# Kernel optimization log

Measured on AMD Instinct MI355X. Metric: run time of the kernel, lower is better.

The kernel has to match this reference:

```python
import jax, jax.numpy as jnp
import numpy as np

NUM_HEADS = 8


def _conv1(x, w, b):
    # 1x1x1 Conv3d == per-voxel channel linear map. x: [B,C,D,H,W], w: [O,C], b: [O]
    return jnp.einsum('bcdhw,oc->bodhw', x, w) + b[None, :, None, None, None]


def setup_inputs() -> dict:
    key = jax.random.key(0)
    ks = jax.random.split(key, 7)
    B, C, D, H, W = 1, 64, 16, 16, 16
    s = 0.02
    return {
        'decoder_features': jax.random.normal(ks[0], (B, C, D, H, W), jnp.float32),
        'mae_features': jax.random.normal(ks[1], (B, C, D, H, W), jnp.float32),
        'q_w': jax.random.normal(ks[2], (C, C), jnp.float32) * s,
        'q_b': jnp.zeros((C,), jnp.float32),
        'k_w': jax.random.normal(ks[3], (C, C), jnp.float32) * s,
        'k_b': jnp.zeros((C,), jnp.float32),
        'v_w': jax.random.normal(ks[4], (C, C), jnp.float32) * s,
        'v_b': jnp.zeros((C,), jnp.float32),
        'o_w': jax.random.normal(ks[5], (C, C), jnp.float32) * s,
        'o_b': jnp.zeros((C,), jnp.float32),
    }


def reference(decoder_features, mae_features, q_w, q_b, k_w, k_b, v_w, v_b, o_w, o_b):
    B, C, D, H, W = decoder_features.shape
    nh = NUM_HEADS
    hd = C // nh
    N = D * H * W
    scale = hd ** -0.5

    def split_heads(x):
        # [B,C,D,H,W] -> [B, nh, N, hd]
        return x.reshape(B, nh, hd, N).transpose(0, 1, 3, 2)

    Q = split_heads(_conv1(decoder_features, q_w, q_b))
    K = split_heads(_conv1(mae_features, k_w, k_b))
    V = split_heads(_conv1(mae_features, v_w, v_b))

    attn = jax.nn.softmax(jnp.einsum('bhnc,bhmc->bhnm', Q, K) * scale, axis=-1)
    out = jnp.einsum('bhnm,bhmc->bhnc', attn, V)  # [B, nh, N, hd]
    out = out.transpose(0, 1, 3, 2).reshape(B, C, D, H, W)
    return _conv1(out, o_w, o_b)
```

## Files before the change

kernel.cpp:

```cpp
#include <hip/hip_runtime.h>
#include <hip/hip_bf16.h>
#include <math.h>


#define N_VOX 4096
#define NH 8
#define QSCALE 0.51010813f

typedef unsigned short ushort_t;
typedef __attribute__((ext_vector_type(8))) short bf16x8;
typedef __attribute__((ext_vector_type(16))) float f32x16;

__device__ __forceinline__ unsigned short f2bf(float f) {
  union { float f; unsigned u; } v; v.f = f;
  unsigned r = v.u + 0x7FFFu + ((v.u >> 16) & 1u);
  return (unsigned short)(r >> 16);
}
__device__ __forceinline__ unsigned pk2bf(float a, float b) {
  __hip_bfloat162 h = __float22bfloat162_rn(float2{a, b});
  union { __hip_bfloat162 h; unsigned u; } c; c.h = h;
  return c.u;
}
__device__ __forceinline__ float ex2(float x) { return __builtin_amdgcn_exp2f(x); }

__global__ __launch_bounds__(256) void qkv_pack(
    const float* __restrict__ dec, const float* __restrict__ mae,
    const float* __restrict__ qw, const float* __restrict__ qb_,
    const float* __restrict__ kw, const float* __restrict__ kb,
    const float* __restrict__ vw, const float* __restrict__ vb,
    ushort_t* __restrict__ Qp, ushort_t* __restrict__ Kp,
    ushort_t* __restrict__ Vt, ushort_t* __restrict__ zeroblk) {
  const int bx = blockIdx.x;
  const int n = blockIdx.y * 256 + threadIdx.x;

  if (bx < 8) {
    const int h = bx;
    float x[64];
#pragma unroll
    for (int c = 0; c < 64; ++c) x[c] = dec[c * N_VOX + n];
    float qv[8];
#pragma unroll
    for (int j = 0; j < 8; ++j) {
      const int o = h * 8 + j;
      float a = qb_[o];
#pragma unroll
      for (int c = 0; c < 64; ++c) a = fmaf(x[c], qw[o * 64 + c], a);
      qv[j] = a * QSCALE;
    }
    uint4 pk;
    pk.x = pk2bf(qv[0], qv[1]); pk.y = pk2bf(qv[2], qv[3]);
    pk.z = pk2bf(qv[4], qv[5]); pk.w = pk2bf(qv[6], qv[7]);
    *(uint4*)(Qp + ((size_t)h * N_VOX + n) * 8) = pk;
  } else {
    const int h = bx - 8;
    float x[64];
#pragma unroll
    for (int c = 0; c < 64; ++c) x[c] = mae[c * N_VOX + n];
    float kv[8], vv[8];
#pragma unroll
    for (int j = 0; j < 8; ++j) {
      const int o = h * 8 + j;
      float a = kb[o], b = vb[o];
#pragma unroll
      for (int c = 0; c < 64; ++c) {
        a = fmaf(x[c], kw[o * 64 + c], a);
        b = fmaf(x[c], vw[o * 64 + c], b);
      }
      kv[j] = a; vv[j] = b;
    }
    uint4 pk;
    pk.x = pk2bf(kv[0], kv[1]); pk.y = pk2bf(kv[2], kv[3]);
    pk.z = pk2bf(kv[4], kv[5]); pk.w = pk2bf(kv[6], kv[7]);
    *(uint4*)(Kp + ((size_t)h * N_VOX + n) * 8) = pk;
#pragma unroll
    for (int d = 0; d < 8; ++d)
      Vt[((size_t)(h * 32 + d)) * N_VOX + n] = f2bf(vv[d]);
    Vt[((size_t)(h * 32 + 8)) * N_VOX + n] = 0x3F80;
    if (h == 0 && n < 8) zeroblk[n] = 0;
  }
}

__global__ __launch_bounds__(256, 3) void attn_mfma(
    const ushort_t* __restrict__ Qp, const ushort_t* __restrict__ Kp,
    const ushort_t* __restrict__ Vt, const ushort_t* __restrict__ zeroblk,
    float* __restrict__ o_part, int kps) {
  const int tid = threadIdx.x;
  const int lane = tid & 63;
  const int wave = tid >> 6;
  const int l31 = lane & 31;
  const int lhalf = lane >> 5;
  const int h = blockIdx.y;
  const int ks = blockIdx.z;
  const int qb = blockIdx.x * 256 + wave * 64;

  __shared__ ushort_t P_lds[8][32 * 36];

  bf16x8 qfrag0 = *(const bf16x8*)(Qp + ((size_t)h * N_VOX + qb + l31) * 8);
  bf16x8 qfrag1 = *(const bf16x8*)(Qp + ((size_t)h * N_VOX + qb + 32 + l31) * 8);

  f32x16 zf, acc0, acc1;
#pragma unroll
  for (int i = 0; i < 16; ++i) { zf[i] = 0.f; acc0[i] = 0.f; acc1[i] = 0.f; }

  const ushort_t* KpH = Kp + (size_t)h * N_VOX * 8;
  const ushort_t* VtH = Vt + ((size_t)h * 32 + l31) * N_VOX;
  ushort_t* pb0 = &P_lds[wave * 2 + 0][l31 * 36];
  ushort_t* pb1 = &P_lds[wave * 2 + 1][l31 * 36];

  const int kbeg = ks * kps;
  for (int kk = 0; kk < kps; kk += 32) {
    const int kcur = kbeg + kk;
    const ushort_t* kp = lhalf ? zeroblk : (KpH + (size_t)(kcur + l31) * 8);
    bf16x8 kf = *(const bf16x8*)kp;

    f32x16 s0 = __builtin_amdgcn_mfma_f32_32x32x16_bf16(kf, qfrag0, zf, 0, 0, 0);
    f32x16 s1 = __builtin_amdgcn_mfma_f32_32x32x16_bf16(kf, qfrag1, zf, 0, 0, 0);

    bf16x8 vf0 = *(const bf16x8*)(VtH + kcur + lhalf * 8);
    bf16x8 vf1 = *(const bf16x8*)(VtH + kcur + 16 + lhalf * 8);

#pragma unroll
    for (int G = 0; G < 4; ++G) {
      uint2 w;
      w.x = pk2bf(ex2(s0[G * 4 + 0]), ex2(s0[G * 4 + 1]));
      w.y = pk2bf(ex2(s0[G * 4 + 2]), ex2(s0[G * 4 + 3]));
      *(uint2*)(pb0 + G * 8 + lhalf * 4) = w;
    }
#pragma unroll
    for (int G = 0; G < 4; ++G) {
      uint2 w;
      w.x = pk2bf(ex2(s1[G * 4 + 0]), ex2(s1[G * 4 + 1]));
      w.y = pk2bf(ex2(s1[G * 4 + 2]), ex2(s1[G * 4 + 3]));
      *(uint2*)(pb1 + G * 8 + lhalf * 4) = w;
    }

#pragma unroll
    for (int grp = 0; grp < 2; ++grp) {
      union { bf16x8 v; uint2 u[2]; } p0, p1;
      p0.u[0] = *(const uint2*)(pb0 + grp * 16 + lhalf * 8);
      p0.u[1] = *(const uint2*)(pb0 + grp * 16 + lhalf * 8 + 4);
      p1.u[0] = *(const uint2*)(pb1 + grp * 16 + lhalf * 8);
      p1.u[1] = *(const uint2*)(pb1 + grp * 16 + lhalf * 8 + 4);
      const bf16x8 vf = grp ? vf1 : vf0;
      acc0 = __builtin_amdgcn_mfma_f32_32x32x16_bf16(p0.v, vf, acc0, 0, 0, 0);
      acc1 = __builtin_amdgcn_mfma_f32_32x32x16_bf16(p1.v, vf, acc1, 0, 0, 0);
    }
  }

  if (l31 < 9) {
    float* ob = o_part + ((size_t)(ks * NH + h) * 9 + l31) * N_VOX;
#pragma unroll
    for (int t = 0; t < 2; ++t) {
      const f32x16 a = t ? acc1 : acc0;
      const int qst = qb + t * 32 + 4 * lhalf;
#pragma unroll
      for (int G = 0; G < 4; ++G) {
        float4 v4 = make_float4(a[G * 4 + 0], a[G * 4 + 1], a[G * 4 + 2], a[G * 4 + 3]);
        *(float4*)(ob + qst + 8 * G) = v4;
      }
    }
  }
}

__global__ __launch_bounds__(256) void combine(
    const float* __restrict__ o_part, float* __restrict__ ocomb, int KS) {
  const int t = blockIdx.x * 256 + threadIdx.x;
  const int c = t >> 12, n = t & (N_VOX - 1);
  const int h = c >> 3, d = c & 7;
  float so = 0.f, sl = 0.f;
  for (int s = 0; s < KS; ++s) {
    const float* base = o_part + ((size_t)(s * NH + h) * 9) * N_VOX;
    so += base[d * N_VOX + n];
    sl += base[8 * N_VOX + n];
  }
  ocomb[(size_t)c * N_VOX + n] = so / sl;
}

__global__ __launch_bounds__(256) void out_proj(
    const float* __restrict__ ocomb, const float* __restrict__ ow,
    const float* __restrict__ obias, float* __restrict__ out) {
  const int og = blockIdx.x;
  const int n = blockIdx.y * 256 + threadIdx.x;
  float x[64];
#pragma unroll
  for (int c = 0; c < 64; ++c) x[c] = ocomb[c * N_VOX + n];
#pragma unroll
  for (int j = 0; j < 8; ++j) {
    const int o = og * 8 + j;
    float acc = obias[o];
#pragma unroll
    for (int c = 0; c < 64; ++c) acc = fmaf(x[c], ow[o * 64 + c], acc);
    out[o * N_VOX + n] = acc;
  }
}

extern "C" void kernel_launch(void* const* d_in, const int* in_sizes, int n_in,
                              void* d_out, int out_size, void* d_ws, size_t ws_size,
                              hipStream_t stream) {
  const float* dec = (const float*)d_in[0];
  const float* mae = (const float*)d_in[1];
  const float* qw = (const float*)d_in[2];
  const float* qb = (const float*)d_in[3];
  const float* kw = (const float*)d_in[4];
  const float* kb = (const float*)d_in[5];
  const float* vw = (const float*)d_in[6];
  const float* vb = (const float*)d_in[7];
  const float* ow = (const float*)d_in[8];
  const float* ob = (const float*)d_in[9];
  float* out = (float*)d_out;
  char* ws = (char*)d_ws;

  const size_t OFF_QP = 0;
  const size_t OFF_KP = 0x80000;
  const size_t OFF_ZERO = 0x100000;
  const size_t OFF_VT = 0x101000;
  const size_t OFF_OPART = 0x301000;

  int KS = 8;
  while (KS > 1) {
    size_t need = OFF_OPART + (size_t)KS * NH * 9 * N_VOX * 4 + 64ull * N_VOX * 4;
    if (need <= ws_size) break;
    KS >>= 1;
  }
  const size_t OFF_OCOMB = OFF_OPART + (size_t)KS * NH * 9 * N_VOX * 4;

  ushort_t* Qp = (ushort_t*)(ws + OFF_QP);
  ushort_t* Kp = (ushort_t*)(ws + OFF_KP);
  ushort_t* zb = (ushort_t*)(ws + OFF_ZERO);
  ushort_t* Vt = (ushort_t*)(ws + OFF_VT);
  float* o_part = (float*)(ws + OFF_OPART);
  float* ocomb = (float*)(ws + OFF_OCOMB);

  qkv_pack<<<dim3(16, 16), 256, 0, stream>>>(dec, mae, qw, qb, kw, kb, vw, vb,
                                             Qp, Kp, Vt, zb);
  attn_mfma<<<dim3(16, 8, KS), 256, 0, stream>>>(Qp, Kp, Vt, zb, o_part,
                                                 N_VOX / KS);
  combine<<<1024, 256, 0, stream>>>(o_part, ocomb, KS);
  out_proj<<<dim3(8, 16), 256, 0, stream>>>(ocomb, ow, ob, out);
}
```

Before: 130.0 us.

## Keep attention probabilities in registers via permlane32 swap instead of LDS

```diff
diff --git a/kernel.cpp b/kernel.cpp
--- a/kernel.cpp
+++ b/kernel.cpp
@@ -22,6 +22,10 @@
   return c.u;
 }
 __device__ __forceinline__ float ex2(float x) { return __builtin_amdgcn_exp2f(x); }
+
+__device__ __forceinline__ void plswap(unsigned& a, unsigned& b) {
+  asm("v_permlane32_swap_b32 %0, %1" : "+v"(a), "+v"(b));
+}
 
 __global__ __launch_bounds__(256) void qkv_pack(
     const float* __restrict__ dec, const float* __restrict__ mae,
@@ -29,7 +33,7 @@
     const float* __restrict__ kw, const float* __restrict__ kb,
     const float* __restrict__ vw, const float* __restrict__ vb,
     ushort_t* __restrict__ Qp, ushort_t* __restrict__ Kp,
-    ushort_t* __restrict__ Vt, ushort_t* __restrict__ zeroblk) {
+    ushort_t* __restrict__ Vt) {
   const int bx = blockIdx.x;
   const int n = blockIdx.y * 256 + threadIdx.x;
 
@@ -76,14 +80,32 @@
     for (int d = 0; d < 8; ++d)
       Vt[((size_t)(h * 32 + d)) * N_VOX + n] = f2bf(vv[d]);
     Vt[((size_t)(h * 32 + 8)) * N_VOX + n] = 0x3F80;
-    if (h == 0 && n < 8) zeroblk[n] = 0;
-  }
-}
-
-__global__ __launch_bounds__(256, 3) void attn_mfma(
+  }
+}
+
+__device__ __forceinline__ f32x16 pv_tile(const f32x16 s, const bf16x8 vf0,
+                                          const bf16x8 vf1, f32x16 acc) {
+#pragma unroll
+  for (int g = 0; g < 2; ++g) {
+    unsigned X0 = pk2bf(ex2(s[g * 8 + 0]), ex2(s[g * 8 + 1]));
+    unsigned X1 = pk2bf(ex2(s[g * 8 + 2]), ex2(s[g * 8 + 3]));
+    unsigned X2 = pk2bf(ex2(s[g * 8 + 4]), ex2(s[g * 8 + 5]));
+    unsigned X3 = pk2bf(ex2(s[g * 8 + 6]), ex2(s[g * 8 + 7]));
+    plswap(X0, X2);
+    plswap(X1, X3);
+    union { unsigned u[4]; bf16x8 v; } pB;
+    pB.u[0] = X0; pB.u[1] = X1; pB.u[2] = X2; pB.u[3] = X3;
+    __builtin_amdgcn_s_setprio(1);
+    acc = __builtin_amdgcn_mfma_f32_32x32x16_bf16(g ? vf1 : vf0, pB.v, acc,
+                                                  0, 0, 0);
+    __builtin_amdgcn_s_setprio(0);
+  }
+  return acc;
+}
+
+__global__ __launch_bounds__(256, 4) void attn_mfma(
     const ushort_t* __restrict__ Qp, const ushort_t* __restrict__ Kp,
-    const ushort_t* __restrict__ Vt, const ushort_t* __restrict__ zeroblk,
-    float* __restrict__ o_part, int kps) {
+    const ushort_t* __restrict__ Vt, float* __restrict__ o_part, int kps) {
   const int tid = threadIdx.x;
   const int lane = tid & 63;
   const int wave = tid >> 6;
@@ -93,8 +115,6 @@
   const int ks = blockIdx.z;
   const int qb = blockIdx.x * 256 + wave * 64;
 
-  __shared__ ushort_t P_lds[8][32 * 36];
-
   bf16x8 qfrag0 = *(const bf16x8*)(Qp + ((size_t)h * N_VOX + qb + l31) * 8);
   bf16x8 qfrag1 = *(const bf16x8*)(Qp + ((size_t)h * N_VOX + qb + 32 + l31) * 8);
 
@@ -104,61 +124,36 @@
 
   const ushort_t* KpH = Kp + (size_t)h * N_VOX * 8;
   const ushort_t* VtH = Vt + ((size_t)h * 32 + l31) * N_VOX;
-  ushort_t* pb0 = &P_lds[wave * 2 + 0][l31 * 36];
-  ushort_t* pb1 = &P_lds[wave * 2 + 1][l31 * 36];
 
   const int kbeg = ks * kps;
   for (int kk = 0; kk < kps; kk += 32) {
     const int kcur = kbeg + kk;
-    const ushort_t* kp = lhalf ? zeroblk : (KpH + (size_t)(kcur + l31) * 8);
-    bf16x8 kf = *(const bf16x8*)kp;
-
-    f32x16 s0 = __builtin_amdgcn_mfma_f32_32x32x16_bf16(kf, qfrag0, zf, 0, 0, 0);
-    f32x16 s1 = __builtin_amdgcn_mfma_f32_32x32x16_bf16(kf, qfrag1, zf, 0, 0, 0);
-
-    bf16x8 vf0 = *(const bf16x8*)(VtH + kcur + lhalf * 8);
-    bf16x8 vf1 = *(const bf16x8*)(VtH + kcur + 16 + lhalf * 8);
-
-#pragma unroll
-    for (int G = 0; G < 4; ++G) {
-      uint2 w;
-      w.x = pk2bf(ex2(s0[G * 4 + 0]), ex2(s0[G * 4 + 1]));
-      w.y = pk2bf(ex2(s0[G * 4 + 2]), ex2(s0[G * 4 + 3]));
-      *(uint2*)(pb0 + G * 8 + lhalf * 4) = w;
-    }
-#pragma unroll
-    for (int G = 0; G < 4; ++G) {
-      uint2 w;
-      w.x = pk2bf(ex2(s1[G * 4 + 0]), ex2(s1[G * 4 + 1]));
-      w.y = pk2bf(ex2(s1[G * 4 + 2]), ex2(s1[G * 4 + 3]));
-      *(uint2*)(pb1 + G * 8 + lhalf * 4) = w;
-    }
-
-#pragma unroll
-    for (int grp = 0; grp < 2; ++grp) {
-      union { bf16x8 v; uint2 u[2]; } p0, p1;
-      p0.u[0] = *(const uint2*)(pb0 + grp * 16 + lhalf * 8);
-      p0.u[1] = *(const uint2*)(pb0 + grp * 16 + lhalf * 8 + 4);
-      p1.u[0] = *(const uint2*)(pb1 + grp * 16 + lhalf * 8);
-      p1.u[1] = *(const uint2*)(pb1 + grp * 16 + lhalf * 8 + 4);
-      const bf16x8 vf = grp ? vf1 : vf0;
-      acc0 = __builtin_amdgcn_mfma_f32_32x32x16_bf16(p0.v, vf, acc0, 0, 0, 0);
-      acc1 = __builtin_amdgcn_mfma_f32_32x32x16_bf16(p1.v, vf, acc1, 0, 0, 0);
-    }
-  }
-
-  if (l31 < 9) {
-    float* ob = o_part + ((size_t)(ks * NH + h) * 9 + l31) * N_VOX;
-#pragma unroll
-    for (int t = 0; t < 2; ++t) {
-      const f32x16 a = t ? acc1 : acc0;
-      const int qst = qb + t * 32 + 4 * lhalf;
-#pragma unroll
-      for (int G = 0; G < 4; ++G) {
-        float4 v4 = make_float4(a[G * 4 + 0], a[G * 4 + 1], a[G * 4 + 2], a[G * 4 + 3]);
-        *(float4*)(ob + qst + 8 * G) = v4;
-      }
-    }
+    bf16x8 kf = {};
+    if (!lhalf) kf = *(const bf16x8*)(KpH + (size_t)(kcur + l31) * 8);
+
+    const bf16x8 vf0 = *(const bf16x8*)(VtH + kcur + lhalf * 8);
+    const bf16x8 vf1 = *(const bf16x8*)(VtH + kcur + 16 + lhalf * 8);
+
+    __builtin_amdgcn_s_setprio(1);
+    const f32x16 s0 = __builtin_amdgcn_mfma_f32_32x32x16_bf16(kf, qfrag0, zf, 0, 0, 0);
+    __builtin_amdgcn_s_setprio(0);
+    acc0 = pv_tile(s0, vf0, vf1, acc0);
+
+    __builtin_amdgcn_s_setprio(1);
+    const f32x16 s1 = __builtin_amdgcn_mfma_f32_32x32x16_bf16(kf, qfrag1, zf, 0, 0, 0);
+    __builtin_amdgcn_s_setprio(0);
+    acc1 = pv_tile(s1, vf0, vf1, acc1);
+  }
+
+  float* ob = o_part + ((size_t)(ks * NH + h) * 9) * N_VOX;
+#pragma unroll
+  for (int t = 0; t < 2; ++t) {
+    const f32x16 a = t ? acc1 : acc0;
+    const int qx = qb + t * 32 + l31;
+#pragma unroll
+    for (int r = 0; r < 4; ++r)
+      ob[(size_t)(r + 4 * lhalf) * N_VOX + qx] = a[r];
+    if (lhalf == 0) ob[(size_t)8 * N_VOX + qx] = a[4];
   }
 }
 
@@ -212,7 +207,6 @@
 
   const size_t OFF_QP = 0;
   const size_t OFF_KP = 0x80000;
-  const size_t OFF_ZERO = 0x100000;
   const size_t OFF_VT = 0x101000;
   const size_t OFF_OPART = 0x301000;
 
@@ -226,14 +220,13 @@
 
   ushort_t* Qp = (ushort_t*)(ws + OFF_QP);
   ushort_t* Kp = (ushort_t*)(ws + OFF_KP);
-  ushort_t* zb = (ushort_t*)(ws + OFF_ZERO);
   ushort_t* Vt = (ushort_t*)(ws + OFF_VT);
   float* o_part = (float*)(ws + OFF_OPART);
   float* ocomb = (float*)(ws + OFF_OCOMB);
 
   qkv_pack<<<dim3(16, 16), 256, 0, stream>>>(dec, mae, qw, qb, kw, kb, vw, vb,
-                                             Qp, Kp, Vt, zb);
-  attn_mfma<<<dim3(16, 8, KS), 256, 0, stream>>>(Qp, Kp, Vt, zb, o_part,
+                                             Qp, Kp, Vt);
+  attn_mfma<<<dim3(16, 8, KS), 256, 0, stream>>>(Qp, Kp, Vt, o_part,
                                                  N_VOX / KS);
   combine<<<1024, 256, 0, stream>>>(o_part, ocomb, KS);
   out_proj<<<dim3(8, 16), 256, 0, stream>>>(ocomb, ow, ob, out);
```

Measured after the change: 134.1 us (median of 2 runs). 1.03x slower.
